# Kernel tuning notes

Measured on AMD Instinct MI355X. Metric: run time of the kernel, lower is better.

## Reference

```python
import jax, jax.numpy as jnp
import numpy as np

N = 256
DIAM = 2.0 * np.pi
VISC = 1e-3
DRAG = 0.1
SCALE = 1.0
PEAK_K = 4
DT = 0.001            # stable_time_step: min(0.001, 0.5*dx/max_velocity) = 0.001 here
NUM_STEPS = 90        # int(T/0.001), T=0.09
RECORD_EVERY = 30
BATCH = 8

# Carpenter-Kennedy low-storage RK4 / Crank-Nicolson tableau (jax-cfd crank_nicolson_rk4)
ALPHAS = (0.0, 0.1496590219993, 0.3704009573644, 0.6222557631345, 0.9582821306748, 1.0)
BETAS = (0.0, -0.4178904745, -1.192151694643, -1.697784692471, -1.514183444257)
GAMMAS = (0.1496590219993, 0.3792103129999, 0.8229550293869, 0.6994504559488, 0.1530572479681)


def _consts():
    kx = jnp.fft.fftfreq(N, d=DIAM / N).astype(jnp.float32)      # cycles / unit length
    ky = jnp.fft.rfftfreq(N, d=DIAM / N).astype(jnp.float32)
    KX, KY = jnp.meshgrid(kx, ky, indexing='ij')                 # [N, N//2+1]
    lap = -(2.0 * np.pi) ** 2 * (KX ** 2 + KY ** 2)              # (2*pi*i*k)^2, real
    lap_nz = lap.at[0, 0].set(1.0)
    # 2/3-rule brick wall dealiasing filter
    third = N // 3
    filt = jnp.zeros((N, N // 2 + 1), jnp.float32)
    filt = filt.at[:third, :third + 1].set(1.0)
    filt = filt.at[-third:, :third + 1].set(1.0)
    # Kolmogorov forcing u=(scale*sin(k y), 0) -> vorticity forcing -scale*k*cos(k y)
    y = (jnp.arange(N, dtype=jnp.float32) + 0.5) * (DIAM / N)    # cell centers
    f = -SCALE * PEAK_K * jnp.cos(PEAK_K * y)[None, :] * jnp.ones((N, 1), jnp.float32)
    f_hat = jnp.fft.rfft2(f)                                     # [N, N//2+1] complex
    return KX, KY, lap, lap_nz, filt, f_hat


def setup_inputs() -> dict:
    key = jax.random.key(0)
    w = jax.random.normal(key, (BATCH, N, N), jnp.float32)
    # band-pass around peak wavenumber to mimic a smooth initial vorticity field
    kx = jnp.fft.fftfreq(N, d=1.0 / N)
    ky = jnp.fft.rfftfreq(N, d=1.0 / N)
    kk = jnp.sqrt(kx[:, None] ** 2 + ky[None, :] ** 2)
    amp = jnp.exp(-0.5 * ((kk - PEAK_K) / 2.0) ** 2).astype(jnp.float32)
    w = jnp.fft.irfft2(jnp.fft.rfft2(w) * amp, s=(N, N))
    w = 5.0 * w / jnp.max(jnp.abs(w))
    return {"vort_init": w.astype(jnp.float32)}


def reference(vort_init) -> jnp.ndarray:
    KX, KY, lap, lap_nz, filt, f_hat = _consts()
    lin = VISC * lap - DRAG                 # implicit (linear) operator symbol, real
    two_pi_i = 2j * jnp.pi

    def explicit(w_hat):
        # vorticity -> velocity via streamfunction
        psi_hat = -w_hat / lap_nz
        vx = jnp.fft.irfft2(two_pi_i * KY * psi_hat, s=(N, N))
        vy = jnp.fft.irfft2(-two_pi_i * KX * psi_hat, s=(N, N))
        gx = jnp.fft.irfft2(two_pi_i * KX * w_hat, s=(N, N))
        gy = jnp.fft.irfft2(two_pi_i * KY * w_hat, s=(N, N))
        adv_hat = jnp.fft.rfft2(-(vx * gx + vy * gy)) * filt   # dealiased advection
        return adv_hat + f_hat

    @jax.checkpoint
    def step(w_hat):
        u = w_hat
        h = jnp.zeros_like(w_hat)
        for k in range(5):
            h = explicit(u) + BETAS[k] * h
            mu = 0.5 * DT * (ALPHAS[k + 1] - ALPHAS[k])
            u = (u + GAMMAS[k] * DT * h + mu * lin * u) / (1.0 - mu * lin)
        return u

    def body(u, _):
        u = step(u)
        return u, u

    w0 = jnp.fft.rfft2(vort_init)                    # [B, N, N//2+1]
    _, traj = jax.lax.scan(body, w0, None, length=NUM_STEPS)
    rec = traj[RECORD_EVERY - 1::RECORD_EVERY]       # [3, B, N, N//2+1]
    return jnp.fft.irfft2(rec, s=(N, N))             # [3, B, N, N]
```

## Files before the change

### kernel.cpp

```cpp
#include <hip/hip_runtime.h>
#include <math.h>

#define PI_F 3.14159265358979323846f
typedef unsigned long long u64;

__constant__ float c_beta[5] = {0.0f, -0.4178904745f, -1.192151694643f,
                                -1.697784692471f, -1.514183444257f};
__constant__ float c_gdt[5]  = {1.496590219993e-4f, 3.792103129999e-4f,
                                8.229550293869e-4f, 6.994504559488e-4f,
                                1.530572479681e-4f};
__constant__ float c_mu[5]   = {7.482951099965e-5f, 1.1037096768255e-4f,
                                1.2592740288505e-4f, 1.6801318377015e-4f,
                                2.08589346626e-5f};

struct __align__(128) Line { int v; int pad[31]; };

struct SharedMem {
  float sAr[1024], sAi[1024], sBr[1024], sBi[1024];
  float twr[128], twi[128];
  float t0r[430], t0i[430], t1r[430], t1i[430];
};

__device__ __forceinline__ float2 ldc(const float2* p)
{
  u64 v = __hip_atomic_load((const u64*)p, __ATOMIC_RELAXED, __HIP_MEMORY_SCOPE_AGENT);
  float2 f; __builtin_memcpy(&f, &v, 8); return f;
}
__device__ __forceinline__ void stg(float2* p, float2 f) { *p = f; }

__device__ __forceinline__ void bar_all(Line* arr, int n, int idx, int gen)
{
  __syncthreads();
  if (threadIdx.x == 0)
    __hip_atomic_store(&arr[idx].v, gen, __ATOMIC_RELAXED, __HIP_MEMORY_SCOPE_AGENT);
  if (threadIdx.x < 64) {
    bool done = false;
    while (!done) {
      bool ok = true;
      for (int w = threadIdx.x; w < n; w += 64)
        if (__hip_atomic_load(&arr[w].v, __ATOMIC_RELAXED, __HIP_MEMORY_SCOPE_AGENT) < gen)
          ok = false;
      done = __all(ok);
      if (!done) __builtin_amdgcn_s_sleep(2);
    }
    __builtin_amdgcn_sched_barrier(0);
  }
  __syncthreads();
}

__device__ __forceinline__ void bar_sync(Line* arr, Line* rel, int n, int idx,
                                         bool lead, int gen, bool fenced)
{
  const int t = threadIdx.x;
  __syncthreads();
  if (t == 0) {
    __builtin_amdgcn_s_waitcnt(0);
    __builtin_amdgcn_sched_barrier(0);
    if (fenced)
      __hip_atomic_store(&arr[idx].v, gen, __ATOMIC_RELEASE, __HIP_MEMORY_SCOPE_AGENT);
    else
      __hip_atomic_store(&arr[idx].v, gen, __ATOMIC_RELAXED, __HIP_MEMORY_SCOPE_AGENT);
  }
  if (lead && t < 64) {
    bool done = false;
    while (!done) {
      bool ok = true;
      for (int w = t; w < n; w += 64)
        if (__hip_atomic_load(&arr[w].v, __ATOMIC_RELAXED, __HIP_MEMORY_SCOPE_AGENT) < gen)
          ok = false;
      done = __all(ok);
      if (!done) __builtin_amdgcn_s_sleep(1);
    }
    __builtin_amdgcn_sched_barrier(0);
    if (fenced)
      (void)__hip_atomic_load(&arr[t & 7].v, __ATOMIC_ACQUIRE, __HIP_MEMORY_SCOPE_AGENT);
    if (t < 8) {
      if (fenced)
        __hip_atomic_store(&rel[t].v, gen, __ATOMIC_RELEASE, __HIP_MEMORY_SCOPE_AGENT);
      else
        __hip_atomic_store(&rel[t].v, gen, __ATOMIC_RELAXED, __HIP_MEMORY_SCOPE_AGENT);
    }
  }
  if (t == 0) {
    Line* f = &rel[idx & 7];
    while (__hip_atomic_load(&f->v, __ATOMIC_RELAXED, __HIP_MEMORY_SCOPE_AGENT) < gen)
      __builtin_amdgcn_s_sleep(1);
    if (fenced)
      (void)__hip_atomic_load(&f->v, __ATOMIC_ACQUIRE, __HIP_MEMORY_SCOPE_AGENT);
    __builtin_amdgcn_sched_barrier(0);
  }
  __syncthreads();
}

template<int B, bool INVERSE>
__device__ __forceinline__ void fftB(SharedMem& sh, int t)
{
  float *sr = sh.sAr, *si = sh.sAi, *dr = sh.sBr, *di = sh.sBi;
#pragma unroll
  for (int s = 0; s < 8; s += 2) {
    __syncthreads();
    const int m  = 1 << s;
    const int k  = t & (m - 1);
    const int e  = (t >> s) & 1;
    const int p  = (t >> (s + 1)) & 1;
    const int q0 = (t >> (s + 2)) << s;
    const int i0 = q0 + k;
    const float w1r = sh.twr[q0];
    const float w1i = INVERSE ? -sh.twi[q0] : sh.twi[q0];
    const float w2r = sh.twr[q0 << 1];
    const float w2i = INVERSE ? -sh.twi[q0 << 1] : sh.twi[q0 << 1];
#pragma unroll
    for (int f = 0; f < B; ++f) {
      const int base = f * 256;
      float S0r = sr[base + i0],       S0i = si[base + i0];
      float S1r = sr[base + i0 + 128], S1i = si[base + i0 + 128];
      float S2r = sr[base + i0 + 64],  S2i = si[base + i0 + 64];
      float S3r = sr[base + i0 + 192], S3i = si[base + i0 + 192];
      float Ar, Ai, Br, Bi;
      if (e == 0) { Ar = S0r + S1r; Ai = S0i + S1i; Br = S2r + S3r; Bi = S2i + S3i; }
      else {
        float xr = S0r - S1r, xi = S0i - S1i;
        Ar = xr * w1r - xi * w1i; Ai = xr * w1i + xi * w1r;
        float yr = S2r - S3r, yi = S2i - S3i;
        float tr = yr * w1r - yi * w1i, ti = yr * w1i + yi * w1r;
        Br = INVERSE ? -ti : ti; Bi = INVERSE ? tr : -tr;
      }
      float Or, Oi;
      if (p == 0) { Or = Ar + Br; Oi = Ai + Bi; }
      else {
        float xr = Ar - Br, xi = Ai - Bi;
        Or = xr * w2r - xi * w2i; Oi = xr * w2i + xi * w2r;
      }
      dr[base + t] = Or; di[base + t] = Oi;
    }
    float* tp;
    tp = sr; sr = dr; dr = tp;
    tp = si; si = di; di = tp;
  }
  __syncthreads();
}

template<int B, bool INVERSE>
__device__ __forceinline__ void fft_reg(SharedMem& sh, int t,
                                        float (&vr)[4], float (&vi)[4])
{
  const int f  = t >> 6;
  const int tt = t & 63;
  const bool act = (f < B);
  __syncthreads();
#pragma unroll
  for (int s4 = 0; s4 < 4; ++s4) {
    const int s = s4 * 2;
    float o_r[4], o_i[4];
    int pos0 = 0;
    if (act) {
      const int k  = tt & ((1 << s) - 1);
      const int q0 = tt - k;
      const float w1r = sh.twr[q0];
      const float w1i = INVERSE ? -sh.twi[q0] : sh.twi[q0];
      const float w2r = sh.twr[q0 << 1];
      const float w2i = INVERSE ? -sh.twi[q0 << 1] : sh.twi[q0 << 1];
      float Ar  = vr[0] + vr[2], Ai  = vi[0] + vi[2];
      float dr_ = vr[0] - vr[2], di_ = vi[0] - vi[2];
      float Atr = dr_ * w1r - di_ * w1i, Ati = dr_ * w1i + di_ * w1r;
      float Br  = vr[1] + vr[3], Bi  = vi[1] + vi[3];
      float er_ = vr[1] - vr[3], ei_ = vi[1] - vi[3];
      float tr_ = er_ * w1r - ei_ * w1i, ti_ = er_ * w1i + ei_ * w1r;
      float Btr = INVERSE ? -ti_ : ti_;
      float Bti = INVERSE ?  tr_ : -tr_;
      o_r[0] = Ar + Br;   o_i[0] = Ai + Bi;
      o_r[1] = Atr + Btr; o_i[1] = Ati + Bti;
      float c0r = Ar - Br,   c0i = Ai - Bi;
      float c1r = Atr - Btr, c1i = Ati - Bti;
      o_r[2] = c0r * w2r - c0i * w2i; o_i[2] = c0r * w2i + c0i * w2r;
      o_r[3] = c1r * w2r - c1i * w2i; o_i[3] = c1r * w2i + c1i * w2r;
      pos0 = ((tt >> s) << (s + 2)) + k;
    }
    if (s4 < 3) {
      float* br_ = (s4 & 1) ? sh.sBr : sh.sAr;
      float* bi_ = (s4 & 1) ? sh.sBi : sh.sAi;
      if (act) {
#pragma unroll
        for (int m = 0; m < 4; ++m) {
          br_[f * 256 + pos0 + (m << s)] = o_r[m];
          bi_[f * 256 + pos0 + (m << s)] = o_i[m];
        }
      }
      __syncthreads();
      if (act) {
#pragma unroll
        for (int j = 0; j < 4; ++j) {
          vr[j] = br_[f * 256 + tt + 64 * j];
          vi[j] = bi_[f * 256 + tt + 64 * j];
        }
      }
    } else if (act) {
#pragma unroll
      for (int j = 0; j < 4; ++j) { vr[j] = o_r[j]; vi[j] = o_i[j]; }
    }
  }
}


__device__ __forceinline__ void stage_tiles(SharedMem& sh, int t, int b, int x0,
    int q0_, int q1_, const float2* __restrict__ G)
{
  for (int i = t; i < 344; i += 256) {
    int ky = i >> 2, xl = i & 3;
    float2 a = ldc(&G[(((size_t)q0_ * 8 + b) * 129 + ky) * 256 + x0 + xl]);
    float2 c = ldc(&G[(((size_t)q1_ * 8 + b) * 129 + ky) * 256 + x0 + xl]);
    sh.t0r[ky * 5 + xl] = a.x; sh.t0i[ky * 5 + xl] = a.y;
    sh.t1r[ky * 5 + xl] = c.x; sh.t1i[ky * 5 + xl] = c.y;
  }
}

__device__ __forceinline__ void build_Z(SharedMem& sh, int f, int tt,
                                        float (&zr)[4], float (&zi)[4])
{
#pragma unroll
  for (int j = 0; j < 4; ++j) {
    int n = tt + 64 * j;
    bool low = (n <= 128);
    int kk = low ? n : 256 - n;
    float ar = 0.f, ai = 0.f, br = 0.f, bi = 0.f;
    if (kk <= 85) {
      ar = sh.t0r[kk * 5 + f]; ai = sh.t0i[kk * 5 + f];
      br = sh.t1r[kk * 5 + f]; bi = sh.t1i[kk * 5 + f];
    }
    zr[j] = low ? (ar - bi) : (ar + bi);
    zi[j] = low ? (ai + br) : (br - ai);
  }
}

__device__ __forceinline__ void real_item4_reg(SharedMem& sh, int t, int b, int x0,
    const float2* __restrict__ G, float2* __restrict__ NL1)
{
  const int f = t >> 6, tt = t & 63;
  __syncthreads();
  stage_tiles(sh, t, b, x0, 0, 1, G);
  __syncthreads();
  float zr[4], zi[4];
  build_Z(sh, f, tt, zr, zi);
  fft_reg<4, true>(sh, t, zr, zi);
  float vx[4], vy[4];
#pragma unroll
  for (int j = 0; j < 4; ++j) { vx[j] = zr[j]; vy[j] = zi[j]; }
  stage_tiles(sh, t, b, x0, 2, 3, G);
  __syncthreads();
  build_Z(sh, f, tt, zr, zi);
  fft_reg<4, true>(sh, t, zr, zi);
  float nl[4];
#pragma unroll
  for (int j = 0; j < 4; ++j) nl[j] = -(vx[j] * zr[j] + vy[j] * zi[j]);
  __syncthreads();
#pragma unroll
  for (int j = 0; j < 4; ++j) sh.sAr[f * 256 + tt + 64 * j] = nl[j];
  __syncthreads();
  float wr2[4], wi2[4];
  if (f < 2) {
#pragma unroll
    for (int j = 0; j < 4; ++j) {
      wr2[j] = sh.sAr[(2 * f) * 256 + tt + 64 * j];
      wi2[j] = sh.sAr[(2 * f + 1) * 256 + tt + 64 * j];
    }
  }
  fft_reg<2, false>(sh, t, wr2, wi2);
  if (f < 2) {
#pragma unroll
    for (int j = 0; j < 4; ++j) {
      sh.sBr[f * 256 + tt + 64 * j] = wr2[j];
      sh.sBi[f * 256 + tt + 64 * j] = wi2[j];
    }
  }
  __syncthreads();
  if (t <= 85) {
    int mI = (256 - t) & 255;
#pragma unroll
    for (int p = 0; p < 2; ++p) {
      float zr_ = sh.sBr[p * 256 + t],  zi_ = sh.sBi[p * 256 + t];
      float wr_ = sh.sBr[p * 256 + mI], wi_ = sh.sBi[p * 256 + mI];
      stg(&NL1[((size_t)b * 86 + t) * 256 + x0 + 2 * p],
          make_float2(0.5f * (zr_ + wr_), 0.5f * (zi_ - wi_)));
      stg(&NL1[((size_t)b * 86 + t) * 256 + x0 + 2 * p + 1],
          make_float2(0.5f * (zi_ + wi_), 0.5f * (wr_ - zr_)));
    }
  }
}

__device__ __forceinline__ void spectral_item4_reg(SharedMem& sh, int t, int b, int ky0,
    const float2* __restrict__ NL1, float2* __restrict__ u, float2* __restrict__ h,
    float2* __restrict__ G, float2* __restrict__ rec,
    float beta, float gdt, float mu, bool doUpdate, int recIdx)
{
  const int f = t >> 6, tt = t & 63;
  const int ky  = ky0 + f;
  const int kyc = (ky > 85) ? 85 : ky;
  const size_t urow = ((size_t)b * 129 + ky) * 256;
  float ur_[4], ui_[4];
#pragma unroll
  for (int j = 0; j < 4; ++j) {
    float2 uu = u[urow + tt + 64 * j];
    ur_[j] = uu.x; ui_[j] = uu.y;
  }

  if (doUpdate) {
    float ar[4], ai[4];
#pragma unroll
    for (int j = 0; j < 4; ++j) {
      float2 nv = ldc(&NL1[((size_t)b * 86 + kyc) * 256 + tt + 64 * j]);
      ar[j] = nv.x; ai[j] = nv.y;
    }
    fft_reg<4, false>(sh, t, ar, ai);
#pragma unroll
    for (int j = 0; j < 4; ++j) {
      const int kx = tt + 64 * j;
      const bool keep = (kx < 85) || (kx >= 171);
      float advr = keep ? ar[j] : 0.f;
      float advi = keep ? ai[j] : 0.f;
      if (kx == 0 && ky == 4) {
        float s_, c_;
        __sincosf(PI_F / 64.0f, &s_, &c_);
        advr -= 131072.0f * c_;
        advi -= 131072.0f * s_;
      }
      float hr = advr, hi = advi;
      if (beta != 0.0f) {
        float2 hh = h[urow + kx];
        hr += beta * hh.x; hi += beta * hh.y;
      }
      const int jx = (kx < 128) ? kx : kx - 256;
      const float k2   = (float)(jx * jx + ky * ky);
      const float lin  = -0.001f * k2 - 0.1f;
      const float anum = 1.0f + mu * lin;
      const float invd = 1.0f / (1.0f - mu * lin);
      ur_[j] = (ur_[j] * anum + gdt * hr) * invd;
      ui_[j] = (ui_[j] * anum + gdt * hi) * invd;
      u[urow + kx] = make_float2(ur_[j], ui_[j]);
      h[urow + kx] = make_float2(hr, hi);
      if (recIdx >= 0)
        stg(&rec[((size_t)recIdx * 8 + b) * (129 * 256) + (size_t)ky * 256 + kx],
            make_float2(ur_[j], ui_[j]));
    }
  }

  const float NRM = 1.0f / 65536.0f;
  const float fjy = (float)ky;
#pragma unroll
  for (int q = 0; q < 4; ++q) {
    float xr[4], xi[4];
#pragma unroll
    for (int j = 0; j < 4; ++j) {
      const int kx = tt + 64 * j;
      const int jx = (kx < 128) ? kx : kx - 256;
      const float fjx = (float)jx;
      const float k2 = (float)(jx * jx + ky * ky);
      const float inv_lapnz = (k2 == 0.0f) ? 1.0f : (-1.0f / k2);
      const float urN = ur_[j] * NRM, uiN = ui_[j] * NRM;
      const float psr = -urN * inv_lapnz, psi_ = -uiN * inv_lapnz;
      if      (q == 0) { xr[j] = -fjy * psi_; xi[j] =  fjy * psr; }
      else if (q == 1) { xr[j] =  fjx * psi_; xi[j] = -fjx * psr; }
      else if (q == 2) { xr[j] = -fjx * uiN;  xi[j] =  fjx * urN; }
      else             { xr[j] = -fjy * uiN;  xi[j] =  fjy * urN; }
    }
    fft_reg<4, true>(sh, t, xr, xi);
#pragma unroll
    for (int j = 0; j < 4; ++j)
      stg(&G[(((size_t)q * 8 + b) * 129 + ky) * 256 + tt + 64 * j],
          make_float2(xr[j], xi[j]));
  }
}

__global__ __launch_bounds__(256, 2) void k_persist(
    const float* __restrict__ vort, float* __restrict__ out,
    float2* __restrict__ u, float2* __restrict__ h,
    float2* __restrict__ G, float2* __restrict__ NL1, float2* __restrict__ rec,
    Line* __restrict__ bar)
{
  const int t   = threadIdx.x;
  const int blk = blockIdx.x;
  const int NBg = gridDim.x;

  Line* arrGrid = bar;
  Line* relGrid = bar + 1024;
  Line* arrGrpA = bar + 1032;
  Line* relGrpA = bar + 1032 + 2048;
  Line* regL    = bar + 1032 + 2048 + 64;

  __shared__ SharedMem sh;
  __shared__ int s_x, s_wi;

  if (t < 128) {
    float s_, c_;
    __sincosf(-(2.0f * PI_F / 256.0f) * (float)t, &s_, &c_);
    sh.twr[t] = c_; sh.twi[t] = s_;
  }

  if (t == 0) {
    int x;
    asm volatile("s_getreg_b32 %0, hwreg(HW_REG_XCC_ID)" : "=s"(x));
    x &= 15;
    s_x  = x;
    s_wi = atomicAdd(&regL[x].v, 1);
  }
  __syncthreads();

  int gen = 0;
  bar_sync(arrGrid, relGrid, NBg, blk, blk == 0, ++gen, true);

  int tot = 0, mn = 1 << 30, mx = 0;
  for (int i = 0; i < 8; ++i) {
    int c = regL[i].v;
    tot += c; mn = min(mn, c); mx = max(mx, c);
  }
  const bool fast = (tot == NBg) && (mn > 0) && (mx <= 256);
  int g, wi, nW;
  if (fast) { g = s_x;     wi = s_wi;     nW = regL[g].v; }
  else      { g = blk & 7; wi = blk >> 3; nW = NBg >> 3;  }
  Line* arr = arrGrpA + g * 256;
  Line* rel = relGrpA + g * 8;
  const bool lead = (wi == 0);

#define GBAR() do { ++gen; if (fast) bar_all(arr, nW, wi, gen); \
                    else bar_sync(arr, rel, nW, wi, lead, gen, true); } while (0)

  float2* W1 = rec + (size_t)g * (129 * 256);
  for (int w = wi; w < 64; w += nW) {
    const int x0 = w * 4;
#pragma unroll
    for (int p = 0; p < 2; ++p) {
      sh.sAr[p * 256 + t] = vort[((size_t)g * 256 + x0 + 2 * p) * 256 + t];
      sh.sAi[p * 256 + t] = vort[((size_t)g * 256 + x0 + 2 * p + 1) * 256 + t];
    }
    fftB<2, false>(sh, t);
    if (t < 129) {
      int mI = (256 - t) & 255;
#pragma unroll
      for (int p = 0; p < 2; ++p) {
        float zr = sh.sAr[p * 256 + t],  zi = sh.sAi[p * 256 + t];
        float wr = sh.sAr[p * 256 + mI], wi2 = sh.sAi[p * 256 + mI];
        stg(&W1[(size_t)t * 256 + x0 + 2 * p],
            make_float2(0.5f * (zr + wr), 0.5f * (zi - wi2)));
        stg(&W1[(size_t)t * 256 + x0 + 2 * p + 1],
            make_float2(0.5f * (zi + wi2), 0.5f * (wr - zr)));
      }
    }
    __syncthreads();
  }
  GBAR();

  for (int w = wi; w < 43; w += nW) {
    const int ky0 = w * 2;
#pragma unroll
    for (int f = 0; f < 2; ++f) {
      float2 v = ldc(&W1[(size_t)(ky0 + f) * 256 + t]);
      sh.sAr[f * 256 + t] = v.x; sh.sAi[f * 256 + t] = v.y;
    }
    fftB<2, false>(sh, t);
#pragma unroll
    for (int f = 0; f < 2; ++f)
      u[((size_t)g * 129 + ky0 + f) * 256 + t] =
        make_float2(sh.sAr[f * 256 + t], sh.sAi[f * 256 + t]);
  }
  for (int w = wi; w < 22; w += nW)
    spectral_item4_reg(sh, t, g, w * 4, NL1, u, h, G, rec, 0.f, 0.f, 0.f, false, -1);

  for (int step = 1; step <= 90; ++step) {
    for (int k = 0; k < 5; ++k) {
      GBAR();
      for (int w = wi; w < 64; w += nW)
        real_item4_reg(sh, t, g, w * 4, G, NL1);
      GBAR();
      const int recIdx = (k == 4 && step % 30 == 0) ? (step / 30 - 1) : -1;
      for (int w = wi; w < 22; w += nW)
        spectral_item4_reg(sh, t, g, w * 4, NL1, u, h, G, rec,
                           c_beta[k], c_gdt[k], c_mu[k], true, recIdx);
    }
  }
  GBAR();

  for (int w = wi; w < 129; w += nW) {
#pragma unroll
    for (int j = 0; j < 2; ++j) {
      int idx = w * 2 + j, r = idx / 86, ky = idx % 86;
      float2 v = ldc(&rec[(((size_t)r * 8 + g) * 129 + ky) * 256 + t]);
      sh.sAr[j * 256 + t] = v.x; sh.sAi[j * 256 + t] = v.y;
    }
    fftB<2, true>(sh, t);
#pragma unroll
    for (int j = 0; j < 2; ++j) {
      int idx = w * 2 + j, r = idx / 86, ky = idx % 86;
      stg(&G[(((size_t)r * 8 + g) * 129 + ky) * 256 + t],
          make_float2(sh.sAr[j * 256 + t], sh.sAi[j * 256 + t]));
    }
  }
  GBAR();

  const float NRM = 1.0f / 65536.0f;
  for (int w = wi; w < 192; w += nW) {
    const int r = w / 64, xh = w % 64, x0 = xh * 4;
    __syncthreads();
    for (int i = t; i < 344; i += 256) {
      int ky = i >> 2, xl = i & 3;
      float2 a = ldc(&G[(((size_t)r * 8 + g) * 129 + ky) * 256 + x0 + xl]);
      sh.t0r[ky * 5 + xl] = a.x; sh.t0i[ky * 5 + xl] = a.y;
    }
    __syncthreads();
    const bool lower = (t <= 128);
    const int  kk    = lower ? t : 256 - t;
#pragma unroll
    for (int f = 0; f < 2; ++f) {
      float ar = 0.f, ai = 0.f, br = 0.f, bi = 0.f;
      if (kk <= 85) {
        ar = sh.t0r[kk * 5 + 2 * f];     ai = sh.t0i[kk * 5 + 2 * f];
        br = sh.t0r[kk * 5 + 2 * f + 1]; bi = sh.t0i[kk * 5 + 2 * f + 1];
      }
      sh.sAr[f * 256 + t] = lower ? (ar - bi) : (ar + bi);
      sh.sAi[f * 256 + t] = lower ? (ai + br) : (br - ai);
    }
    fftB<2, true>(sh, t);
#pragma unroll
    for (int f = 0; f < 2; ++f) {
      out[((((size_t)r * 8 + g) * 256) + x0 + 2 * f) * 256 + t]     = sh.sAr[f * 256 + t] * NRM;
      out[((((size_t)r * 8 + g) * 256) + x0 + 2 * f + 1) * 256 + t] = sh.sAi[f * 256 + t] * NRM;
    }
    __syncthreads();
  }
#undef GBAR
}

extern "C" void kernel_launch(void* const* d_in, const int* in_sizes, int n_in,
                              void* d_out, int out_size, void* d_ws, size_t ws_size,
                              hipStream_t stream)
{
  const float* vort = (const float*)d_in[0];
  float* out = (float*)d_out;

  float2* base = (float2*)d_ws;
  float2* u    = base;
  float2* h    = u + 264192;
  float2* G    = h + 264192;
  float2* NL1  = G + 1056768;
  float2* rec  = NL1 + 176128;
  Line*   bar  = (Line*)(rec + 792576);
  const int nLines = 1024 + 8 + 2048 + 64 + 16;

  hipMemsetAsync(bar, 0, (size_t)nLines * sizeof(Line), stream);

  int maxPerCU = 0;
  hipOccupancyMaxActiveBlocksPerMultiprocessor(&maxPerCU, k_persist, 256, 0);
  int NBg = maxPerCU * 256;
  if (NBg <= 0)  NBg = 512;
  if (NBg > 512) NBg = 512;
  NBg &= ~63;
  if (NBg < 64)  NBg = 64;

  void* args[] = {(void*)&vort, (void*)&out, (void*)&u, (void*)&h,
                  (void*)&G, (void*)&NL1, (void*)&rec, (void*)&bar};
  hipError_t e = hipLaunchCooperativeKernel(k_persist, dim3(NBg), dim3(256),
                                            args, 0, stream);
  if (e != hipSuccess) {
    hipLaunchKernelGGL(k_persist, dim3(NBg), dim3(256), 0, stream,
                       vort, out, u, h, G, NL1, rec, bar);
  }
}
```

Before: 7.359 ms.

## Batch paired FFTs per barrier sequence and swizzle LDS indices

The real-space stage now stages all four gradient tiles at once and runs the two inverse FFTs together in one dual FFT routine. That halves the barrier sequences and gives each thread two independent butterflies of work. The spectral stage changes from four rows per item to two rows per item. Its output FFTs use the same dual routine, while the forward NL FFT now runs with only half the warps active. LDS indices in the register FFT are XOR-swizzled to reduce bank conflicts. In exchange, LDS use roughly doubles and register pressure rises.

```diff
diff --git a/kernel.cpp b/kernel.cpp
--- a/kernel.cpp
+++ b/kernel.cpp
@@ -16,10 +16,13 @@
 struct __align__(128) Line { int v; int pad[31]; };
 
 struct SharedMem {
-  float sAr[1024], sAi[1024], sBr[1024], sBi[1024];
+  float sAr[2048], sAi[2048], sBr[2048], sBi[2048];
   float twr[128], twi[128];
   float t0r[430], t0i[430], t1r[430], t1i[430];
+  float t2r[430], t2i[430], t3r[430], t3i[430];
 };
+
+__device__ __forceinline__ int swz(int i) { return i ^ (i >> 3); }
 
 __device__ __forceinline__ float2 ldc(const float2* p)
 {
@@ -140,6 +143,27 @@
   __syncthreads();
 }
 
+template<bool INVERSE>
+__device__ __forceinline__ void bfly4(const float (&vr)[4], const float (&vi)[4],
+    float w1r, float w1i, float w2r, float w2i,
+    float (&o_r)[4], float (&o_i)[4])
+{
+  float Ar  = vr[0] + vr[2], Ai  = vi[0] + vi[2];
+  float dr_ = vr[0] - vr[2], di_ = vi[0] - vi[2];
+  float Atr = dr_ * w1r - di_ * w1i, Ati = dr_ * w1i + di_ * w1r;
+  float Br  = vr[1] + vr[3], Bi  = vi[1] + vi[3];
+  float er_ = vr[1] - vr[3], ei_ = vi[1] - vi[3];
+  float tr_ = er_ * w1r - ei_ * w1i, ti_ = er_ * w1i + ei_ * w1r;
+  float Btr = INVERSE ? -ti_ : ti_;
+  float Bti = INVERSE ?  tr_ : -tr_;
+  o_r[0] = Ar + Br;   o_i[0] = Ai + Bi;
+  o_r[1] = Atr + Btr; o_i[1] = Ati + Bti;
+  float c0r = Ar - Br,   c0i = Ai - Bi;
+  float c1r = Atr - Btr, c1i = Ati - Bti;
+  o_r[2] = c0r * w2r - c0i * w2i; o_i[2] = c0r * w2i + c0i * w2r;
+  o_r[3] = c1r * w2r - c1i * w2i; o_i[3] = c1r * w2i + c1i * w2r;
+}
+
 template<int B, bool INVERSE>
 __device__ __forceinline__ void fft_reg(SharedMem& sh, int t,
                                         float (&vr)[4], float (&vi)[4])
@@ -160,38 +184,25 @@
       const float w1i = INVERSE ? -sh.twi[q0] : sh.twi[q0];
       const float w2r = sh.twr[q0 << 1];
       const float w2i = INVERSE ? -sh.twi[q0 << 1] : sh.twi[q0 << 1];
-      float Ar  = vr[0] + vr[2], Ai  = vi[0] + vi[2];
-      float dr_ = vr[0] - vr[2], di_ = vi[0] - vi[2];
-      float Atr = dr_ * w1r - di_ * w1i, Ati = dr_ * w1i + di_ * w1r;
-      float Br  = vr[1] + vr[3], Bi  = vi[1] + vi[3];
-      float er_ = vr[1] - vr[3], ei_ = vi[1] - vi[3];
-      float tr_ = er_ * w1r - ei_ * w1i, ti_ = er_ * w1i + ei_ * w1r;
-      float Btr = INVERSE ? -ti_ : ti_;
-      float Bti = INVERSE ?  tr_ : -tr_;
-      o_r[0] = Ar + Br;   o_i[0] = Ai + Bi;
-      o_r[1] = Atr + Btr; o_i[1] = Ati + Bti;
-      float c0r = Ar - Br,   c0i = Ai - Bi;
-      float c1r = Atr - Btr, c1i = Ati - Bti;
-      o_r[2] = c0r * w2r - c0i * w2i; o_i[2] = c0r * w2i + c0i * w2r;
-      o_r[3] = c1r * w2r - c1i * w2i; o_i[3] = c1r * w2i + c1i * w2r;
+      bfly4<INVERSE>(vr, vi, w1r, w1i, w2r, w2i, o_r, o_i);
       pos0 = ((tt >> s) << (s + 2)) + k;
     }
     if (s4 < 3) {
-      float* br_ = (s4 & 1) ? sh.sBr : sh.sAr;
-      float* bi_ = (s4 & 1) ? sh.sBi : sh.sAi;
+      float* xr = (s4 & 1) ? sh.sBr : sh.sAr;
+      float* xi = (s4 & 1) ? sh.sBi : sh.sAi;
       if (act) {
 #pragma unroll
         for (int m = 0; m < 4; ++m) {
-          br_[f * 256 + pos0 + (m << s)] = o_r[m];
-          bi_[f * 256 + pos0 + (m << s)] = o_i[m];
+          const int w_ = f * 256 + swz(pos0 + (m << s));
+          xr[w_] = o_r[m]; xi[w_] = o_i[m];
         }
       }
       __syncthreads();
       if (act) {
 #pragma unroll
         for (int j = 0; j < 4; ++j) {
-          vr[j] = br_[f * 256 + tt + 64 * j];
-          vi[j] = bi_[f * 256 + tt + 64 * j];
+          const int rd = f * 256 + swz(tt + 64 * j);
+          vr[j] = xr[rd]; vi[j] = xi[rd];
         }
       }
     } else if (act) {
@@ -201,21 +212,57 @@
   }
 }
 
-
-__device__ __forceinline__ void stage_tiles(SharedMem& sh, int t, int b, int x0,
-    int q0_, int q1_, const float2* __restrict__ G)
-{
-  for (int i = t; i < 344; i += 256) {
-    int ky = i >> 2, xl = i & 3;
-    float2 a = ldc(&G[(((size_t)q0_ * 8 + b) * 129 + ky) * 256 + x0 + xl]);
-    float2 c = ldc(&G[(((size_t)q1_ * 8 + b) * 129 + ky) * 256 + x0 + xl]);
-    sh.t0r[ky * 5 + xl] = a.x; sh.t0i[ky * 5 + xl] = a.y;
-    sh.t1r[ky * 5 + xl] = c.x; sh.t1i[ky * 5 + xl] = c.y;
-  }
-}
-
-__device__ __forceinline__ void build_Z(SharedMem& sh, int f, int tt,
-                                        float (&zr)[4], float (&zi)[4])
+template<bool INVERSE>
+__device__ __forceinline__ void fft_reg_dual(SharedMem& sh, int t,
+    float (&ar)[4], float (&ai)[4], float (&br)[4], float (&bi)[4])
+{
+  const int f  = t >> 6;
+  const int tt = t & 63;
+  __syncthreads();
+#pragma unroll
+  for (int s4 = 0; s4 < 4; ++s4) {
+    const int s = s4 * 2;
+    const int k  = tt & ((1 << s) - 1);
+    const int q0 = tt - k;
+    const float w1r = sh.twr[q0];
+    const float w1i = INVERSE ? -sh.twi[q0] : sh.twi[q0];
+    const float w2r = sh.twr[q0 << 1];
+    const float w2i = INVERSE ? -sh.twi[q0 << 1] : sh.twi[q0 << 1];
+    float oAr[4], oAi[4], oBr[4], oBi[4];
+    bfly4<INVERSE>(ar, ai, w1r, w1i, w2r, w2i, oAr, oAi);
+    bfly4<INVERSE>(br, bi, w1r, w1i, w2r, w2i, oBr, oBi);
+    if (s4 < 3) {
+      const int pos0 = ((tt >> s) << (s + 2)) + k;
+      float* xr = (s4 & 1) ? sh.sBr : sh.sAr;
+      float* xi = (s4 & 1) ? sh.sBi : sh.sAi;
+      const int baseA = f * 256, baseB = (f + 4) * 256;
+#pragma unroll
+      for (int m = 0; m < 4; ++m) {
+        const int w_ = swz(pos0 + (m << s));
+        xr[baseA + w_] = oAr[m]; xi[baseA + w_] = oAi[m];
+        xr[baseB + w_] = oBr[m]; xi[baseB + w_] = oBi[m];
+      }
+      __syncthreads();
+#pragma unroll
+      for (int j = 0; j < 4; ++j) {
+        const int rd = swz(tt + 64 * j);
+        ar[j] = xr[baseA + rd]; ai[j] = xi[baseA + rd];
+        br[j] = xr[baseB + rd]; bi[j] = xi[baseB + rd];
+      }
+    } else {
+#pragma unroll
+      for (int j = 0; j < 4; ++j) {
+        ar[j] = oAr[j]; ai[j] = oAi[j];
+        br[j] = oBr[j]; bi[j] = oBi[j];
+      }
+    }
+  }
+}
+
+
+__device__ __forceinline__ void build_Z2(const float* t0r_, const float* t0i_,
+    const float* t1r_, const float* t1i_, int f, int tt,
+    float (&zr)[4], float (&zi)[4])
 {
 #pragma unroll
   for (int j = 0; j < 4; ++j) {
@@ -224,8 +271,8 @@
     int kk = low ? n : 256 - n;
     float ar = 0.f, ai = 0.f, br = 0.f, bi = 0.f;
     if (kk <= 85) {
-      ar = sh.t0r[kk * 5 + f]; ai = sh.t0i[kk * 5 + f];
-      br = sh.t1r[kk * 5 + f]; bi = sh.t1i[kk * 5 + f];
+      ar = t0r_[kk * 5 + f]; ai = t0i_[kk * 5 + f];
+      br = t1r_[kk * 5 + f]; bi = t1i_[kk * 5 + f];
     }
     zr[j] = low ? (ar - bi) : (ar + bi);
     zi[j] = low ? (ai + br) : (br - ai);
@@ -237,21 +284,26 @@
 {
   const int f = t >> 6, tt = t & 63;
   __syncthreads();
-  stage_tiles(sh, t, b, x0, 0, 1, G);
-  __syncthreads();
-  float zr[4], zi[4];
-  build_Z(sh, f, tt, zr, zi);
-  fft_reg<4, true>(sh, t, zr, zi);
-  float vx[4], vy[4];
-#pragma unroll
-  for (int j = 0; j < 4; ++j) { vx[j] = zr[j]; vy[j] = zi[j]; }
-  stage_tiles(sh, t, b, x0, 2, 3, G);
-  __syncthreads();
-  build_Z(sh, f, tt, zr, zi);
-  fft_reg<4, true>(sh, t, zr, zi);
+  for (int i = t; i < 344; i += 256) {
+    int ky = i >> 2, xl = i & 3;
+    float2 a0 = ldc(&G[(((size_t)0 * 8 + b) * 129 + ky) * 256 + x0 + xl]);
+    float2 a1 = ldc(&G[(((size_t)1 * 8 + b) * 129 + ky) * 256 + x0 + xl]);
+    float2 a2 = ldc(&G[(((size_t)2 * 8 + b) * 129 + ky) * 256 + x0 + xl]);
+    float2 a3 = ldc(&G[(((size_t)3 * 8 + b) * 129 + ky) * 256 + x0 + xl]);
+    sh.t0r[ky * 5 + xl] = a0.x; sh.t0i[ky * 5 + xl] = a0.y;
+    sh.t1r[ky * 5 + xl] = a1.x; sh.t1i[ky * 5 + xl] = a1.y;
+    sh.t2r[ky * 5 + xl] = a2.x; sh.t2i[ky * 5 + xl] = a2.y;
+    sh.t3r[ky * 5 + xl] = a3.x; sh.t3i[ky * 5 + xl] = a3.y;
+  }
+  __syncthreads();
+  float ar_[4], ai_[4], br_[4], bi_[4];
+  build_Z2(sh.t0r, sh.t0i, sh.t1r, sh.t1i, f, tt, ar_, ai_);
+  build_Z2(sh.t2r, sh.t2i, sh.t3r, sh.t3i, f, tt, br_, bi_);
+  fft_reg_dual<true>(sh, t, ar_, ai_, br_, bi_);
   float nl[4];
 #pragma unroll
-  for (int j = 0; j < 4; ++j) nl[j] = -(vx[j] * zr[j] + vy[j] * zi[j]);
+  for (int j = 0; j < 4; ++j)
+    nl[j] = -(ar_[j] * br_[j] + ai_[j] * bi_[j]);
   __syncthreads();
 #pragma unroll
   for (int j = 0; j < 4; ++j) sh.sAr[f * 256 + tt + 64 * j] = nl[j];
@@ -287,86 +339,107 @@
   }
 }
 
-__device__ __forceinline__ void spectral_item4_reg(SharedMem& sh, int t, int b, int ky0,
+__device__ __forceinline__ void spectral_item2_reg(SharedMem& sh, int t, int b, int ky0,
     const float2* __restrict__ NL1, float2* __restrict__ u, float2* __restrict__ h,
     float2* __restrict__ G, float2* __restrict__ rec,
     float beta, float gdt, float mu, bool doUpdate, int recIdx)
 {
   const int f = t >> 6, tt = t & 63;
-  const int ky  = ky0 + f;
-  const int kyc = (ky > 85) ? 85 : ky;
-  const size_t urow = ((size_t)b * 129 + ky) * 256;
-  float ur_[4], ui_[4];
-#pragma unroll
-  for (int j = 0; j < 4; ++j) {
-    float2 uu = u[urow + tt + 64 * j];
-    ur_[j] = uu.x; ui_[j] = uu.y;
-  }
+  const size_t r0 = ((size_t)b * 129 + ky0) * 256;
 
   if (doUpdate) {
     float ar[4], ai[4];
-#pragma unroll
-    for (int j = 0; j < 4; ++j) {
-      float2 nv = ldc(&NL1[((size_t)b * 86 + kyc) * 256 + tt + 64 * j]);
-      ar[j] = nv.x; ai[j] = nv.y;
-    }
-    fft_reg<4, false>(sh, t, ar, ai);
-#pragma unroll
-    for (int j = 0; j < 4; ++j) {
-      const int kx = tt + 64 * j;
-      const bool keep = (kx < 85) || (kx >= 171);
-      float advr = keep ? ar[j] : 0.f;
-      float advi = keep ? ai[j] : 0.f;
-      if (kx == 0 && ky == 4) {
-        float s_, c_;
-        __sincosf(PI_F / 64.0f, &s_, &c_);
-        advr -= 131072.0f * c_;
-        advi -= 131072.0f * s_;
-      }
-      float hr = advr, hi = advi;
-      if (beta != 0.0f) {
-        float2 hh = h[urow + kx];
-        hr += beta * hh.x; hi += beta * hh.y;
-      }
-      const int jx = (kx < 128) ? kx : kx - 256;
-      const float k2   = (float)(jx * jx + ky * ky);
-      const float lin  = -0.001f * k2 - 0.1f;
-      const float anum = 1.0f + mu * lin;
-      const float invd = 1.0f / (1.0f - mu * lin);
-      ur_[j] = (ur_[j] * anum + gdt * hr) * invd;
-      ui_[j] = (ui_[j] * anum + gdt * hi) * invd;
-      u[urow + kx] = make_float2(ur_[j], ui_[j]);
-      h[urow + kx] = make_float2(hr, hi);
-      if (recIdx >= 0)
-        stg(&rec[((size_t)recIdx * 8 + b) * (129 * 256) + (size_t)ky * 256 + kx],
-            make_float2(ur_[j], ui_[j]));
-    }
+    if (f < 2) {
+#pragma unroll
+      for (int j = 0; j < 4; ++j) {
+        float2 nv = ldc(&NL1[((size_t)b * 86 + ky0 + f) * 256 + tt + 64 * j]);
+        ar[j] = nv.x; ai[j] = nv.y;
+      }
+    }
+    fft_reg<2, false>(sh, t, ar, ai);
+    if (f < 2) {
+      const int ky = ky0 + f;
+      const size_t row = r0 + (size_t)f * 256;
+#pragma unroll
+      for (int j = 0; j < 4; ++j) {
+        const int kx = tt + 64 * j;
+        const bool keep = (kx < 85) || (kx >= 171);
+        float advr = keep ? ar[j] : 0.f;
+        float advi = keep ? ai[j] : 0.f;
+        if (kx == 0 && ky == 4) {
+          float s_, c_;
+          __sincosf(PI_F / 64.0f, &s_, &c_);
+          advr -= 131072.0f * c_;
+          advi -= 131072.0f * s_;
+        }
+        float hr = advr, hi = advi;
+        if (beta != 0.0f) {
+          float2 hh = h[row + kx];
+          hr += beta * hh.x; hi += beta * hh.y;
+        }
+        const int jx = (kx < 128) ? kx : kx - 256;
+        const float k2   = (float)(jx * jx + ky * ky);
+        const float lin  = -0.001f * k2 - 0.1f;
+        const float anum = 1.0f + mu * lin;
+        const float invd = 1.0f / (1.0f - mu * lin);
+        float2 uu = u[row + kx];
+        float urv = (uu.x * anum + gdt * hr) * invd;
+        float uiv = (uu.y * anum + gdt * hi) * invd;
+        u[row + kx] = make_float2(urv, uiv);
+        h[row + kx] = make_float2(hr, hi);
+        if (recIdx >= 0)
+          stg(&rec[((size_t)recIdx * 8 + b) * (129 * 256) + (size_t)ky * 256 + kx],
+              make_float2(urv, uiv));
+      }
+    }
+    __syncthreads();
+  }
+
+  float u0r[4], u0i[4], u1r[4], u1i[4];
+#pragma unroll
+  for (int j = 0; j < 4; ++j) {
+    float2 a = u[r0 + tt + 64 * j];
+    float2 c = u[r0 + 256 + tt + 64 * j];
+    u0r[j] = a.x; u0i[j] = a.y; u1r[j] = c.x; u1i[j] = c.y;
   }
 
   const float NRM = 1.0f / 65536.0f;
-  const float fjy = (float)ky;
-#pragma unroll
-  for (int q = 0; q < 4; ++q) {
-    float xr[4], xi[4];
-#pragma unroll
-    for (int j = 0; j < 4; ++j) {
-      const int kx = tt + 64 * j;
-      const int jx = (kx < 128) ? kx : kx - 256;
-      const float fjx = (float)jx;
-      const float k2 = (float)(jx * jx + ky * ky);
-      const float inv_lapnz = (k2 == 0.0f) ? 1.0f : (-1.0f / k2);
-      const float urN = ur_[j] * NRM, uiN = ui_[j] * NRM;
-      const float psr = -urN * inv_lapnz, psi_ = -uiN * inv_lapnz;
-      if      (q == 0) { xr[j] = -fjy * psi_; xi[j] =  fjy * psr; }
-      else if (q == 1) { xr[j] =  fjx * psi_; xi[j] = -fjx * psr; }
-      else if (q == 2) { xr[j] = -fjx * uiN;  xi[j] =  fjx * urN; }
-      else             { xr[j] = -fjy * uiN;  xi[j] =  fjy * urN; }
-    }
-    fft_reg<4, true>(sh, t, xr, xi);
-#pragma unroll
-    for (int j = 0; j < 4; ++j)
-      stg(&G[(((size_t)q * 8 + b) * 129 + ky) * 256 + tt + 64 * j],
-          make_float2(xr[j], xi[j]));
+  const float fy0 = (float)ky0, fy1 = (float)(ky0 + 1);
+  float x0r[4], x0i[4], x1r[4], x1i[4];
+#pragma unroll
+  for (int j = 0; j < 4; ++j) {
+    const int kx = tt + 64 * j;
+    const int jx = (kx < 128) ? kx : kx - 256;
+    const float fjx = (float)jx;
+    {
+      const float k2 = (float)(jx * jx + ky0 * ky0);
+      const float il = (k2 == 0.f) ? 1.f : (-1.f / k2);
+      const float urN = u0r[j] * NRM, uiN = u0i[j] * NRM;
+      const float psr = -urN * il, psi_ = -uiN * il;
+      if      (f == 0) { x0r[j] = -fy0 * psi_; x0i[j] =  fy0 * psr; }
+      else if (f == 1) { x0r[j] =  fjx * psi_; x0i[j] = -fjx * psr; }
+      else if (f == 2) { x0r[j] = -fjx * uiN;  x0i[j] =  fjx * urN; }
+      else             { x0r[j] = -fy0 * uiN;  x0i[j] =  fy0 * urN; }
+    }
+    {
+      const int ky1 = ky0 + 1;
+      const float k2 = (float)(jx * jx + ky1 * ky1);
+      const float il = (k2 == 0.f) ? 1.f : (-1.f / k2);
+      const float urN = u1r[j] * NRM, uiN = u1i[j] * NRM;
+      const float psr = -urN * il, psi_ = -uiN * il;
+      if      (f == 0) { x1r[j] = -fy1 * psi_; x1i[j] =  fy1 * psr; }
+      else if (f == 1) { x1r[j] =  fjx * psi_; x1i[j] = -fjx * psr; }
+      else if (f == 2) { x1r[j] = -fjx * uiN;  x1i[j] =  fjx * urN; }
+      else             { x1r[j] = -fy1 * uiN;  x1i[j] =  fy1 * urN; }
+    }
+  }
+  fft_reg_dual<true>(sh, t, x0r, x0i, x1r, x1i);
+#pragma unroll
+  for (int j = 0; j < 4; ++j) {
+    stg(&G[(((size_t)f * 8 + b) * 129 + ky0) * 256 + tt + 64 * j],
+        make_float2(x0r[j], x0i[j]));
+    stg(&G[(((size_t)f * 8 + b) * 129 + ky0 + 1) * 256 + tt + 64 * j],
+        make_float2(x1r[j], x1i[j]));
   }
 }
 
@@ -461,8 +534,8 @@
       u[((size_t)g * 129 + ky0 + f) * 256 + t] =
         make_float2(sh.sAr[f * 256 + t], sh.sAi[f * 256 + t]);
   }
-  for (int w = wi; w < 22; w += nW)
-    spectral_item4_reg(sh, t, g, w * 4, NL1, u, h, G, rec, 0.f, 0.f, 0.f, false, -1);
+  for (int w = wi; w < 43; w += nW)
+    spectral_item2_reg(sh, t, g, w * 2, NL1, u, h, G, rec, 0.f, 0.f, 0.f, false, -1);
 
   for (int step = 1; step <= 90; ++step) {
     for (int k = 0; k < 5; ++k) {
@@ -471,8 +544,8 @@
         real_item4_reg(sh, t, g, w * 4, G, NL1);
       GBAR();
       const int recIdx = (k == 4 && step % 30 == 0) ? (step / 30 - 1) : -1;
-      for (int w = wi; w < 22; w += nW)
-        spectral_item4_reg(sh, t, g, w * 4, NL1, u, h, G, rec,
+      for (int w = wi; w < 43; w += nW)
+        spectral_item2_reg(sh, t, g, w * 2, NL1, u, h, G, rec,
                            c_beta[k], c_gdt[k], c_mu[k], true, recIdx);
     }
   }
```

After: 7.701 ms. 4.6% more time.
